# Kernel optimization log

Measured on AMD Instinct MI355X. Metric: run time of the kernel, lower is better.

Reference implementation:

```python
import jax, jax.numpy as jnp
import numpy as np

HIDDEN = 1024
N_HEADS = 16
D_HEAD = HIDDEN // N_HEADS
B, S = 4, 2048


def setup_inputs() -> dict:
    key = jax.random.key(0)
    ks = jax.random.split(key, 7)
    scale = 1.0 / np.sqrt(D_HEAD)
    return {
        "sequences": jax.random.normal(ks[0], (B, S, HIDDEN), dtype=jnp.float32),
        "Wq": jax.random.normal(ks[1], (N_HEADS, D_HEAD, D_HEAD), dtype=jnp.float32) * scale,
        "bq": jax.random.normal(ks[2], (N_HEADS, D_HEAD), dtype=jnp.float32) * 0.02,
        "Wk": jax.random.normal(ks[3], (N_HEADS, D_HEAD, D_HEAD), dtype=jnp.float32) * scale,
        "bk": jax.random.normal(ks[4], (N_HEADS, D_HEAD), dtype=jnp.float32) * 0.02,
        "Wv": jax.random.normal(ks[5], (N_HEADS, D_HEAD, D_HEAD), dtype=jnp.float32) * scale,
        "bv": jax.random.normal(ks[6], (N_HEADS, D_HEAD), dtype=jnp.float32) * 0.02,
    }


def reference(sequences, Wq, bq, Wk, bk, Wv, bv):
    # sequences: [B, S, hidden]; split hidden into per-head slices -> [B, S, H, d]
    x = sequences.reshape(B, S, N_HEADS, D_HEAD)
    # per-head Linear: y = x @ W^T + b (torch nn.Linear convention)
    q = jnp.einsum("bshd,hed->bshe", x, Wq) + bq  # [B,S,H,d]
    k = jnp.einsum("bshd,hed->bshe", x, Wk) + bk
    v = jnp.einsum("bshd,hed->bshe", x, Wv) + bv
    scores = jnp.einsum("bqhd,bkhd->bhqk", q, k) / np.sqrt(D_HEAD)  # [B,H,S,S]
    attn = jax.nn.softmax(scores, axis=-1)
    out = jnp.einsum("bhqk,bkhd->bqhd", attn, v)  # [B,S,H,d]
    # hstack over heads == concat along feature dim
    return out.reshape(B, S, HIDDEN)
```

## Files before the change

kernel.cpp:

```cpp
#include <hip/hip_runtime.h>
#include <hip/hip_bf16.h>

#define NB 4
#define NS 2048
#define NH 16
#define ND 64
#define NHID 1024
#define NT (NS / 64)
#define QSCALE 0.18033688011112042f

typedef __bf16 bf16x8 __attribute__((ext_vector_type(8)));
typedef _Float16 f16x8 __attribute__((ext_vector_type(8)));
typedef _Float16 f16x4 __attribute__((ext_vector_type(4)));
typedef __fp16 h16x2 __attribute__((ext_vector_type(2)));
typedef float f32x4 __attribute__((ext_vector_type(4)));

#define GLDS16(g, l)                                                      \
  __builtin_amdgcn_global_load_lds(                                       \
      (const __attribute__((address_space(1))) void*)(g),                 \
      (__attribute__((address_space(3))) void*)(l), 16, 0, 0)

__device__ __forceinline__ bf16x8 cvt8(const float* __restrict__ p) {
  float4 f0 = *(const float4*)p;
  float4 f1 = *(const float4*)(p + 4);
  bf16x8 v;
  v[0] = (__bf16)f0.x; v[1] = (__bf16)f0.y; v[2] = (__bf16)f0.z; v[3] = (__bf16)f0.w;
  v[4] = (__bf16)f1.x; v[5] = (__bf16)f1.y; v[6] = (__bf16)f1.z; v[7] = (__bf16)f1.w;
  return v;
}

__device__ __forceinline__ bf16x8 cvt8s(const float* __restrict__ p, float s) {
  float4 f0 = *(const float4*)p;
  float4 f1 = *(const float4*)(p + 4);
  bf16x8 v;
  v[0] = (__bf16)(f0.x * s); v[1] = (__bf16)(f0.y * s);
  v[2] = (__bf16)(f0.z * s); v[3] = (__bf16)(f0.w * s);
  v[4] = (__bf16)(f1.x * s); v[5] = (__bf16)(f1.y * s);
  v[6] = (__bf16)(f1.z * s); v[7] = (__bf16)(f1.w * s);
  return v;
}

__global__ __launch_bounds__(256, 2) void qkv_proj(
    const float* __restrict__ x,
    const float* __restrict__ Wq, const float* __restrict__ Wk,
    const float* __restrict__ Wv,
    const float* __restrict__ bq, const float* __restrict__ bk,
    const float* __restrict__ bv,
    __bf16* __restrict__ qs, __bf16* __restrict__ ks, _Float16* __restrict__ vt)
{
  __shared__ __align__(16) unsigned short tiles[4][64 * 72];

  const int bid = blockIdx.x;
  const int hg = bid & 3;
  const int s0 = ((bid >> 2) & 31) * 64;
  const int b  = bid >> 7;
  const int tid  = threadIdx.x;
  const int w    = tid >> 6;
  const int lane = tid & 63;
  const int l16  = lane & 15;
  const int quad = lane >> 4;
  const int h  = hg * 4 + w;
  const int bh = b * NH + h;

  unsigned short* tile = tiles[w];
  __bf16*   tb16 = (__bf16*)tile;
  _Float16* tf16 = (_Float16*)tile;

  bf16x8 aX[4][2];
#pragma unroll
  for (int tb = 0; tb < 4; ++tb) {
    const float* xrow = x + ((size_t)(b * NS + s0 + tb * 16 + l16)) * NHID + h * ND;
#pragma unroll
    for (int k2 = 0; k2 < 2; ++k2)
      aX[tb][k2] = cvt8(xrow + k2 * 32 + quad * 8);
  }

#pragma unroll
  for (int mat = 0; mat < 3; ++mat) {
    const float* Wm = ((mat == 0) ? Wq : (mat == 1) ? Wk : Wv) + (size_t)h * ND * ND;
    const float* bm = (mat == 0) ? bq : (mat == 1) ? bk : bv;
    const float wsc = (mat == 0) ? QSCALE : 1.0f;

    f32x4 acc[4][4];
#pragma unroll
    for (int nb = 0; nb < 4; ++nb) {
      const int e = nb * 16 + l16;
      bf16x8 w0 = cvt8s(Wm + e * ND + quad * 8, wsc);
      bf16x8 w1 = cvt8s(Wm + e * ND + 32 + quad * 8, wsc);
#pragma unroll
      for (int tbk = 0; tbk < 4; ++tbk) {
        f32x4 a = {0.f, 0.f, 0.f, 0.f};
        a = __builtin_amdgcn_mfma_f32_16x16x32_bf16(aX[tbk][0], w0, a, 0, 0, 0);
        a = __builtin_amdgcn_mfma_f32_16x16x32_bf16(aX[tbk][1], w1, a, 0, 0, 0);
        acc[nb][tbk] = a;
      }
    }

    if (mat < 2) {
#pragma unroll
      for (int nb = 0; nb < 4; ++nb) {
        float bias = bm[h * ND + nb * 16 + l16] * wsc;
#pragma unroll
        for (int tbk = 0; tbk < 4; ++tbk)
#pragma unroll
          for (int r = 0; r < 4; ++r)
            tb16[(tbk * 16 + quad * 4 + r) * 72 + nb * 16 + l16] =
                (__bf16)(acc[nb][tbk][r] + bias);
      }
#pragma unroll
      for (int p = 0; p < 8; ++p) {
        int idx = p * 64 + lane, row = idx >> 3, c = idx & 7;
        bf16x8 v8 = *(const bf16x8*)(tb16 + row * 72 + c * 8);
        if (mat == 0)
          *(bf16x8*)(qs + ((size_t)bh * NS + s0 + row) * ND + c * 8) = v8;
        else
          *(bf16x8*)(ks + ((size_t)bh * NS + s0 + row) * ND + ((c ^ (row & 7)) * 8)) = v8;
      }
    } else {
#pragma unroll
      for (int nb = 0; nb < 4; ++nb) {
        float bias = bm[h * ND + nb * 16 + l16];
#pragma unroll
        for (int tbk = 0; tbk < 4; ++tbk) {
          union { h16x2 h2[2]; uint2 u2; } pv;
          pv.h2[0] = __builtin_amdgcn_cvt_pkrtz(acc[nb][tbk][0] + bias,
                                                acc[nb][tbk][1] + bias);
          pv.h2[1] = __builtin_amdgcn_cvt_pkrtz(acc[nb][tbk][2] + bias,
                                                acc[nb][tbk][3] + bias);
          *(uint2*)&tf16[(nb * 16 + l16) * 72 + tbk * 16 + quad * 4] = pv.u2;
        }
      }
#pragma unroll
      for (int p = 0; p < 8; ++p) {
        int idx = p * 64 + lane, row = idx >> 3, c = idx & 7;
        int K0 = 32 * (c >> 2) + 4 * (c & 3);
        union { f16x4 v4[2]; f16x8 v8; } u;
        u.v4[0] = *(const f16x4*)(tf16 + row * 72 + K0);
        u.v4[1] = *(const f16x4*)(tf16 + row * 72 + K0 + 16);
        *(f16x8*)(vt + ((size_t)bh * ND + row) * NS + s0 + ((c ^ (row & 7)) * 8)) = u.v8;
      }
    }
  }
}

__global__ __launch_bounds__(256, 2) void attn(
    const __bf16* __restrict__ qs, const __bf16* __restrict__ ks,
    const _Float16* __restrict__ vt, float* __restrict__ out)
{
  __shared__ __align__(16) __bf16   KT[2][64 * 64];
  __shared__ __align__(16) _Float16 VT[2][64 * 64];

  const int bid = blockIdx.x;
  const int qt = bid >> 6;
  const int h  = bid & 15;
  const int b  = (bid >> 4) & 3;
  const int bh = b * NH + h;
  const int tid  = threadIdx.x;
  const int w    = tid >> 6;
  const int lane = tid & 63;
  const int l16  = lane & 15;
  const int quad = lane >> 4;
  const int swz  = l16 & 7;
  const int qw   = qt * 256 + w * 64;

  const __bf16*   Kb = ks + (size_t)bh * NS * ND;
  const _Float16* Vb = vt + (size_t)bh * ND * NS;

  bf16x8 Qf[4][2];
#pragma unroll
  for (int qb = 0; qb < 4; ++qb)
#pragma unroll
    for (int k2 = 0; k2 < 2; ++k2)
      Qf[qb][k2] = *(const bf16x8*)(qs + ((size_t)bh * NS + qw + qb * 16 + l16) * ND +
                                    k2 * 32 + quad * 8);

  f32x4 acc[4][4];
#pragma unroll
  for (int qb = 0; qb < 4; ++qb)
#pragma unroll
    for (int mb = 0; mb < 4; ++mb) acc[qb][mb] = (f32x4){0.f, 0.f, 0.f, 0.f};
  f32x4 lacc[4];
#pragma unroll
  for (int qb = 0; qb < 4; ++qb) lacc[qb] = (f32x4){0.f, 0.f, 0.f, 0.f};
  const f16x8 onesf = {(_Float16)1.f, (_Float16)1.f, (_Float16)1.f, (_Float16)1.f,
                       (_Float16)1.f, (_Float16)1.f, (_Float16)1.f, (_Float16)1.f};

#pragma unroll
  for (int p = 0; p < 2; ++p) {
    int i = (w * 2 + p) * 64 + lane;
    GLDS16(Kb + (size_t)0 * 4096 + i * 8, &KT[0][i * 8]);
    int row = i >> 3, cc = i & 7;
    GLDS16(Vb + (size_t)row * NS + 0 * 64 + cc * 8, &VT[0][i * 8]);
  }

  for (int kt = 0; kt < NT; ++kt) {
    const int cur = kt & 1;
    __syncthreads();
    if (kt + 1 < NT) {
      const int nxt = cur ^ 1;
#pragma unroll
      for (int p = 0; p < 2; ++p) {
        int i = (w * 2 + p) * 64 + lane;
        GLDS16(Kb + (size_t)(kt + 1) * 4096 + i * 8, &KT[nxt][i * 8]);
        int row = i >> 3, cc = i & 7;
        GLDS16(Vb + (size_t)row * NS + (kt + 1) * 64 + cc * 8, &VT[nxt][i * 8]);
      }
    }

    const __bf16*   Kl = KT[cur];
    const _Float16* Vl = VT[cur];

    f32x4 sc[4][4];
    __builtin_amdgcn_s_setprio(1);
#pragma unroll
    for (int kb = 0; kb < 4; ++kb) {
      const __bf16* krow = Kl + (kb * 16 + l16) * 64;
      bf16x8 Kf0 = *(const bf16x8*)(krow + ((quad ^ swz) * 8));
      bf16x8 Kf1 = *(const bf16x8*)(krow + (((4 + quad) ^ swz) * 8));
#pragma unroll
      for (int qb = 0; qb < 4; ++qb) {
        f32x4 s = {0.f, 0.f, 0.f, 0.f};
        s = __builtin_amdgcn_mfma_f32_16x16x32_bf16(Kf0, Qf[qb][0], s, 0, 0, 0);
        s = __builtin_amdgcn_mfma_f32_16x16x32_bf16(Kf1, Qf[qb][1], s, 0, 0, 0);
        sc[qb][kb] = s;
      }
    }
    __builtin_amdgcn_s_setprio(0);

    f16x8 bp8[4][2];
#pragma unroll
    for (int qb = 0; qb < 4; ++qb) {
#pragma unroll
      for (int g = 0; g < 2; ++g) {
        float p0 = __builtin_amdgcn_exp2f(sc[qb][2 * g][0]);
        float p1 = __builtin_amdgcn_exp2f(sc[qb][2 * g][1]);
        float p2 = __builtin_amdgcn_exp2f(sc[qb][2 * g][2]);
        float p3 = __builtin_amdgcn_exp2f(sc[qb][2 * g][3]);
        float p4 = __builtin_amdgcn_exp2f(sc[qb][2 * g + 1][0]);
        float p5 = __builtin_amdgcn_exp2f(sc[qb][2 * g + 1][1]);
        float p6 = __builtin_amdgcn_exp2f(sc[qb][2 * g + 1][2]);
        float p7 = __builtin_amdgcn_exp2f(sc[qb][2 * g + 1][3]);
        union { h16x2 v2[4]; f16x8 v8; } u;
        u.v2[0] = __builtin_amdgcn_cvt_pkrtz(p0, p1);
        u.v2[1] = __builtin_amdgcn_cvt_pkrtz(p2, p3);
        u.v2[2] = __builtin_amdgcn_cvt_pkrtz(p4, p5);
        u.v2[3] = __builtin_amdgcn_cvt_pkrtz(p6, p7);
        bp8[qb][g] = u.v8;
      }
    }

    __builtin_amdgcn_s_setprio(1);
#pragma unroll
    for (int g = 0; g < 2; ++g) {
#pragma unroll
      for (int mb = 0; mb < 4; ++mb) {
        f16x8 Vf = *(const f16x8*)(Vl + (mb * 16 + l16) * 64 + (((g * 4 + quad) ^ swz)) * 8);
#pragma unroll
        for (int qb = 0; qb < 4; ++qb)
          acc[qb][mb] = __builtin_amdgcn_mfma_f32_16x16x32_f16(Vf, bp8[qb][g], acc[qb][mb], 0, 0, 0);
      }
#pragma unroll
      for (int qb = 0; qb < 4; ++qb)
        lacc[qb] = __builtin_amdgcn_mfma_f32_16x16x32_f16(onesf, bp8[qb][g], lacc[qb], 0, 0, 0);
    }
    __builtin_amdgcn_s_setprio(0);
  }

#pragma unroll
  for (int qb = 0; qb < 4; ++qb) {
    float invl = 1.0f / lacc[qb][0];
    const size_t orow = ((size_t)(b * NS) + qw + qb * 16 + l16) * NHID + h * ND;
#pragma unroll
    for (int mb = 0; mb < 4; ++mb) {
      float4 o4 = {acc[qb][mb][0] * invl, acc[qb][mb][1] * invl,
                   acc[qb][mb][2] * invl, acc[qb][mb][3] * invl};
      *(float4*)(out + orow + mb * 16 + quad * 4) = o4;
    }
  }
}

extern "C" void kernel_launch(void* const* d_in, const int* in_sizes, int n_in,
                              void* d_out, int out_size, void* d_ws, size_t ws_size,
                              hipStream_t stream) {
  const float* x  = (const float*)d_in[0];
  const float* Wq = (const float*)d_in[1];
  const float* bq = (const float*)d_in[2];
  const float* Wk = (const float*)d_in[3];
  const float* bk = (const float*)d_in[4];
  const float* Wv = (const float*)d_in[5];
  const float* bv = (const float*)d_in[6];
  float* out = (float*)d_out;

  const size_t per = (size_t)NB * NH * NS * ND;
  __bf16* qs   = (__bf16*)d_ws;
  __bf16* ksb  = qs + per;
  _Float16* vt = (_Float16*)(ksb + per);

  qkv_proj<<<NB * (NS / 64) * (NH / 4), 256, 0, stream>>>(
      x, Wq, Wk, Wv, bq, bk, bv, qs, ksb, vt);
  attn<<<8 * NB * NH, 256, 0, stream>>>(qs, ksb, vt, out);
}
```

Baseline: 172.4 us.

## Software-pipeline attention loop: overlap PV MFMAs with next tile's softmax

```diff
diff --git a/kernel.cpp b/kernel.cpp
--- a/kernel.cpp
+++ b/kernel.cpp
@@ -142,6 +142,81 @@
     }
   }
 }
+
+#define STAGE_NEXT(T)                                                          \
+    if ((T) + 1 < NT) {                                                        \
+      const int nxt_ = ((T) + 1) & 1;                                          \
+      _Pragma("unroll")                                                        \
+      for (int p_ = 0; p_ < 2; ++p_) {                                         \
+        int i_ = (w * 2 + p_) * 64 + lane;                                     \
+        GLDS16(Kb + (size_t)((T) + 1) * 4096 + i_ * 8, &KT[nxt_][i_ * 8]);     \
+        int row_ = i_ >> 3, cc_ = i_ & 7;                                      \
+        GLDS16(Vb + (size_t)row_ * NS + ((T) + 1) * 64 + cc_ * 8,              \
+               &VT[nxt_][i_ * 8]);                                             \
+      }                                                                        \
+    }
+
+#define TILE(T, BPOLD, BPNEW, DO_PV)                                           \
+  {                                                                            \
+    const int cur_ = (T) & 1;                                                  \
+    __syncthreads();                                                           \
+    STAGE_NEXT(T);                                                             \
+    const __bf16* Kl_ = KT[cur_];                                              \
+    f32x4 sc_[4][4];                                                           \
+    __builtin_amdgcn_s_setprio(1);                                             \
+    _Pragma("unroll")                                                          \
+    for (int kb_ = 0; kb_ < 4; ++kb_) {                                        \
+      const __bf16* krow_ = Kl_ + (kb_ * 16 + l16) * 64;                       \
+      bf16x8 Kf0_ = *(const bf16x8*)(krow_ + ((quad ^ swz) * 8));              \
+      bf16x8 Kf1_ = *(const bf16x8*)(krow_ + (((4 + quad) ^ swz) * 8));        \
+      _Pragma("unroll")                                                        \
+      for (int qb_ = 0; qb_ < 4; ++qb_) {                                      \
+        f32x4 s_ = {0.f, 0.f, 0.f, 0.f};                                       \
+        s_ = __builtin_amdgcn_mfma_f32_16x16x32_bf16(Kf0_, Qf[qb_][0], s_, 0, 0, 0); \
+        s_ = __builtin_amdgcn_mfma_f32_16x16x32_bf16(Kf1_, Qf[qb_][1], s_, 0, 0, 0); \
+        sc_[qb_][kb_] = s_;                                                    \
+      }                                                                        \
+    }                                                                          \
+    __builtin_amdgcn_s_setprio(0);                                             \
+    if (DO_PV) {                                                               \
+      _Pragma("unroll")                                                        \
+      for (int g_ = 0; g_ < 2; ++g_)                                           \
+        _Pragma("unroll")                                                      \
+        for (int mb_ = 0; mb_ < 4; ++mb_)                                      \
+          _Pragma("unroll")                                                    \
+          for (int qb_ = 0; qb_ < 4; ++qb_)                                    \
+            acc[qb_][mb_] = __builtin_amdgcn_mfma_f32_16x16x32_f16(            \
+                Vreg[g_][mb_], BPOLD[qb_][g_], acc[qb_][mb_], 0, 0, 0);        \
+    }                                                                          \
+    _Pragma("unroll")                                                          \
+    for (int qb_ = 0; qb_ < 4; ++qb_) {                                        \
+      _Pragma("unroll")                                                        \
+      for (int g_ = 0; g_ < 2; ++g_) {                                         \
+        float p0_ = __builtin_amdgcn_exp2f(sc_[qb_][2 * g_][0]);               \
+        float p1_ = __builtin_amdgcn_exp2f(sc_[qb_][2 * g_][1]);               \
+        float p2_ = __builtin_amdgcn_exp2f(sc_[qb_][2 * g_][2]);               \
+        float p3_ = __builtin_amdgcn_exp2f(sc_[qb_][2 * g_][3]);               \
+        float p4_ = __builtin_amdgcn_exp2f(sc_[qb_][2 * g_ + 1][0]);           \
+        float p5_ = __builtin_amdgcn_exp2f(sc_[qb_][2 * g_ + 1][1]);           \
+        float p6_ = __builtin_amdgcn_exp2f(sc_[qb_][2 * g_ + 1][2]);           \
+        float p7_ = __builtin_amdgcn_exp2f(sc_[qb_][2 * g_ + 1][3]);           \
+        lp[qb_] += ((p0_ + p1_) + (p2_ + p3_)) + ((p4_ + p5_) + (p6_ + p7_));  \
+        union { h16x2 v2[4]; f16x8 v8; } u_;                                   \
+        u_.v2[0] = __builtin_amdgcn_cvt_pkrtz(p0_, p1_);                       \
+        u_.v2[1] = __builtin_amdgcn_cvt_pkrtz(p2_, p3_);                       \
+        u_.v2[2] = __builtin_amdgcn_cvt_pkrtz(p4_, p5_);                       \
+        u_.v2[3] = __builtin_amdgcn_cvt_pkrtz(p6_, p7_);                       \
+        BPNEW[qb_][g_] = u_.v8;                                                \
+      }                                                                        \
+    }                                                                          \
+    const _Float16* Vl_ = VT[cur_];                                            \
+    _Pragma("unroll")                                                          \
+    for (int g_ = 0; g_ < 2; ++g_)                                             \
+      _Pragma("unroll")                                                        \
+      for (int mb_ = 0; mb_ < 4; ++mb_)                                        \
+        Vreg[g_][mb_] = *(const f16x8*)(Vl_ + (mb_ * 16 + l16) * 64 +          \
+                                        (((g_ * 4 + quad) ^ swz)) * 8);        \
+  }
 
 __global__ __launch_bounds__(256, 2) void attn(
     const __bf16* __restrict__ qs, const __bf16* __restrict__ ks,
@@ -179,11 +254,10 @@
   for (int qb = 0; qb < 4; ++qb)
 #pragma unroll
     for (int mb = 0; mb < 4; ++mb) acc[qb][mb] = (f32x4){0.f, 0.f, 0.f, 0.f};
-  f32x4 lacc[4];
-#pragma unroll
-  for (int qb = 0; qb < 4; ++qb) lacc[qb] = (f32x4){0.f, 0.f, 0.f, 0.f};
-  const f16x8 onesf = {(_Float16)1.f, (_Float16)1.f, (_Float16)1.f, (_Float16)1.f,
-                       (_Float16)1.f, (_Float16)1.f, (_Float16)1.f, (_Float16)1.f};
+  float lp[4] = {0.f, 0.f, 0.f, 0.f};
+
+  f16x8 bpA[4][2], bpB[4][2];
+  f16x8 Vreg[2][4];
 
 #pragma unroll
   for (int p = 0; p < 2; ++p) {
@@ -193,82 +267,27 @@
     GLDS16(Vb + (size_t)row * NS + 0 * 64 + cc * 8, &VT[0][i * 8]);
   }
 
-  for (int kt = 0; kt < NT; ++kt) {
-    const int cur = kt & 1;
-    __syncthreads();
-    if (kt + 1 < NT) {
-      const int nxt = cur ^ 1;
-#pragma unroll
-      for (int p = 0; p < 2; ++p) {
-        int i = (w * 2 + p) * 64 + lane;
-        GLDS16(Kb + (size_t)(kt + 1) * 4096 + i * 8, &KT[nxt][i * 8]);
-        int row = i >> 3, cc = i & 7;
-        GLDS16(Vb + (size_t)row * NS + (kt + 1) * 64 + cc * 8, &VT[nxt][i * 8]);
-      }
-    }
-
-    const __bf16*   Kl = KT[cur];
-    const _Float16* Vl = VT[cur];
-
-    f32x4 sc[4][4];
-    __builtin_amdgcn_s_setprio(1);
-#pragma unroll
-    for (int kb = 0; kb < 4; ++kb) {
-      const __bf16* krow = Kl + (kb * 16 + l16) * 64;
-      bf16x8 Kf0 = *(const bf16x8*)(krow + ((quad ^ swz) * 8));
-      bf16x8 Kf1 = *(const bf16x8*)(krow + (((4 + quad) ^ swz) * 8));
-#pragma unroll
-      for (int qb = 0; qb < 4; ++qb) {
-        f32x4 s = {0.f, 0.f, 0.f, 0.f};
-        s = __builtin_amdgcn_mfma_f32_16x16x32_bf16(Kf0, Qf[qb][0], s, 0, 0, 0);
-        s = __builtin_amdgcn_mfma_f32_16x16x32_bf16(Kf1, Qf[qb][1], s, 0, 0, 0);
-        sc[qb][kb] = s;
-      }
-    }
-    __builtin_amdgcn_s_setprio(0);
-
-    f16x8 bp8[4][2];
-#pragma unroll
-    for (int qb = 0; qb < 4; ++qb) {
-#pragma unroll
-      for (int g = 0; g < 2; ++g) {
-        float p0 = __builtin_amdgcn_exp2f(sc[qb][2 * g][0]);
-        float p1 = __builtin_amdgcn_exp2f(sc[qb][2 * g][1]);
-        float p2 = __builtin_amdgcn_exp2f(sc[qb][2 * g][2]);
-        float p3 = __builtin_amdgcn_exp2f(sc[qb][2 * g][3]);
-        float p4 = __builtin_amdgcn_exp2f(sc[qb][2 * g + 1][0]);
-        float p5 = __builtin_amdgcn_exp2f(sc[qb][2 * g + 1][1]);
-        float p6 = __builtin_amdgcn_exp2f(sc[qb][2 * g + 1][2]);
-        float p7 = __builtin_amdgcn_exp2f(sc[qb][2 * g + 1][3]);
-        union { h16x2 v2[4]; f16x8 v8; } u;
-        u.v2[0] = __builtin_amdgcn_cvt_pkrtz(p0, p1);
-        u.v2[1] = __builtin_amdgcn_cvt_pkrtz(p2, p3);
-        u.v2[2] = __builtin_amdgcn_cvt_pkrtz(p4, p5);
-        u.v2[3] = __builtin_amdgcn_cvt_pkrtz(p6, p7);
-        bp8[qb][g] = u.v8;
-      }
-    }
-
-    __builtin_amdgcn_s_setprio(1);
-#pragma unroll
-    for (int g = 0; g < 2; ++g) {
-#pragma unroll
-      for (int mb = 0; mb < 4; ++mb) {
-        f16x8 Vf = *(const f16x8*)(Vl + (mb * 16 + l16) * 64 + (((g * 4 + quad) ^ swz)) * 8);
-#pragma unroll
-        for (int qb = 0; qb < 4; ++qb)
-          acc[qb][mb] = __builtin_amdgcn_mfma_f32_16x16x32_f16(Vf, bp8[qb][g], acc[qb][mb], 0, 0, 0);
-      }
+  TILE(0, bpA, bpA, 0);
+  for (int tt = 0; tt < 15; ++tt) {
+    TILE(2 * tt + 1, bpA, bpB, 1);
+    TILE(2 * tt + 2, bpB, bpA, 1);
+  }
+  TILE(31, bpA, bpB, 1);
+#pragma unroll
+  for (int g = 0; g < 2; ++g)
+#pragma unroll
+    for (int mb = 0; mb < 4; ++mb)
 #pragma unroll
       for (int qb = 0; qb < 4; ++qb)
-        lacc[qb] = __builtin_amdgcn_mfma_f32_16x16x32_f16(onesf, bp8[qb][g], lacc[qb], 0, 0, 0);
-    }
-    __builtin_amdgcn_s_setprio(0);
-  }
+        acc[qb][mb] = __builtin_amdgcn_mfma_f32_16x16x32_f16(
+            Vreg[g][mb], bpB[qb][g], acc[qb][mb], 0, 0, 0);
 
 #pragma unroll
   for (int qb = 0; qb < 4; ++qb) {
-    float invl = 1.0f / lacc[qb][0];
+    float ls = lp[qb];
+    ls += __shfl_xor(ls, 16, 64);
+    ls += __shfl_xor(ls, 32, 64);
+    float invl = 1.0f / ls;
     const size_t orow = ((size_t)(b * NS) + qw + qb * 16 + l16) * NHID + h * ND;
 #pragma unroll
     for (int mb = 0; mb < 4; ++mb) {
```

New measurement: 266.0 us. 54.3% more time.
